# Kernel tuning notes

Measured on AMD Instinct MI355X. Metric: run time of the kernel, lower is better.

Reference implementation:

```python
import jax, jax.numpy as jnp
import numpy as np

# ---- static problem config (matches init_kwargs / input_specs) ----
L = 8                      # num_labels
D = H = W = 96             # volume dims
N = D * H * W
ALPHA, BETA, GAMMA = 8.0, 0.125, 3.0
NIT = 5                    # num_iterations
# 4-D bilateral grid dims: 3 spatial axes scaled by alpha, 1 intensity axis scaled by beta
GD = (int(np.ceil((D - 1) / ALPHA)) + 2,
      int(np.ceil((H - 1) / ALPHA)) + 2,
      int(np.ceil((W - 1) / ALPHA)) + 2,
      int(np.ceil(1.0 / BETA)) + 2)
GSIZE = int(np.prod(GD))
_STRIDES = np.array([GD[1] * GD[2] * GD[3], GD[2] * GD[3], GD[3], 1], dtype=np.int32)


def spatial_gaussian(Q):
    """Exact separable 3D Gaussian filter with sigma=GAMMA. Q: (L, D, H, W)."""
    r = int(3 * GAMMA)
    t = jnp.arange(-r, r + 1, dtype=Q.dtype)
    k = jnp.exp(-0.5 * (t / GAMMA) ** 2)
    k = k / k.sum()
    x = Q[None]  # (1, L, D, H, W)
    for ax in range(3):
        kspatial = [1, 1, 1]
        kspatial[ax] = 2 * r + 1
        kern = jnp.broadcast_to(k.reshape([1, 1] + kspatial), [L, 1] + kspatial)
        pad = [(r, r) if i == ax else (0, 0) for i in range(3)]
        x = jax.lax.conv_general_dilated(
            x, kern, (1, 1, 1), pad, feature_group_count=L,
            dimension_numbers=('NCDHW', 'OIDHW', 'NCDHW'))
    return x[0]


def splat_coords(img):
    """4-D lattice features per voxel. img: (D, H, W). Returns lo (4,N) int32, frac (4,N)."""
    zz, yy, xx = jnp.meshgrid(jnp.arange(D, dtype=img.dtype),
                              jnp.arange(H, dtype=img.dtype),
                              jnp.arange(W, dtype=img.dtype), indexing='ij')
    feats = jnp.stack([zz.reshape(-1) / ALPHA,
                       yy.reshape(-1) / ALPHA,
                       xx.reshape(-1) / ALPHA,
                       img.reshape(-1) / BETA], axis=0)  # (4, N)
    hi = jnp.asarray(GD, feats.dtype).reshape(4, 1) - 2.0
    lo_f = jnp.clip(jnp.floor(feats), 0.0, hi)
    frac = feats - lo_f
    return lo_f.astype(jnp.int32), frac


def blur1(g, ax):
    """[1,2,1]/4 blur along axis ax (grid-unit Gaussian of the splat-blur-slice)."""
    pad = [(0, 0)] * g.ndim
    pad[ax] = (1, 1)
    gp = jnp.pad(g, pad)
    n = g.shape[ax]
    a = jax.lax.slice_in_dim(gp, 0, n, axis=ax)
    b = jax.lax.slice_in_dim(gp, 1, n + 1, axis=ax)
    c = jax.lax.slice_in_dim(gp, 2, n + 2, axis=ax)
    return 0.25 * a + 0.5 * b + 0.25 * c


def lattice_filter(vals, lo, frac):
    """Splat-blur-slice high-dim Gaussian filter. vals: (C, N) -> (C, N)."""
    C = vals.shape[0]
    grid = jnp.zeros((C, GSIZE), vals.dtype)
    idxs, ws = [], []
    for bits in range(16):  # 16 corners of the 4-D cell (multilinear splat)
        off = np.array([(bits >> d) & 1 for d in range(4)], dtype=np.int32)
        w = jnp.prod(jnp.where(off[:, None] == 1, frac, 1.0 - frac), axis=0)  # (N,)
        idx = jnp.sum((lo + off[:, None]) * _STRIDES[:, None], axis=0)        # (N,)
        idxs.append(idx)
        ws.append(w)
        grid = grid.at[:, idx].add(vals * w[None])
    g = grid.reshape((C,) + GD)
    for ax in range(1, 5):
        g = blur1(g, ax)
    gf = g.reshape(C, GSIZE)
    out = jnp.zeros_like(vals)
    for bits in range(16):  # slice
        out = out + ws[bits][None] * gf[:, idxs[bits]]
    return out


def bilateral_apply(Q, lo, frac):
    """Normalized bilateral filtering of Q (L, D, H, W)."""
    vals = jnp.concatenate([Q.reshape(L, N), jnp.ones((1, N), Q.dtype)], axis=0)
    out = lattice_filter(vals, lo, frac)
    return (out[:L] / (out[L:] + 1e-8)).reshape(L, D, H, W)


def reference(U, image, spatial_ker_weights, bilateral_ker_weights, compatibility_matrix):
    Us = U[0]                               # (L, D, H, W); batch must be 1
    lo, frac = splat_coords(image[0, 0])    # lattice built once from image (as in __init__)
    Q = Us
    for _ in range(NIT):
        # NOTE: original code recomputes softmax of the (unchanged) unary U each iteration
        Qsm = jax.nn.softmax(Us, axis=0)
        sp = spatial_gaussian(Qsm).reshape(L, -1)
        bi = bilateral_apply(Qsm, lo, frac).reshape(L, -1)
        Qp = compatibility_matrix @ (spatial_ker_weights @ sp + bilateral_ker_weights @ bi)
        Q = Us + Qp.reshape(L, D, H, W)
    return jax.nn.softmax(Q, axis=0)[None]


def setup_inputs() -> dict:
    key = jax.random.key(0)
    k1, k2 = jax.random.split(key)
    U = jax.random.normal(k1, (1, L, D, H, W), jnp.float32)
    image = jax.random.uniform(k2, (1, 1, D, H, W), jnp.float32)
    eye = jnp.eye(L, dtype=jnp.float32)
    return {
        "U": U,
        "image": image,
        "spatial_ker_weights": 3.0 * eye,     # spatial_ker_weight * I
        "bilateral_ker_weights": 10.0 * eye,  # bilateral_ker_weight * I
        "compatibility_matrix": eye,
    }
```

## Files before the change

kernel.cpp:

```cpp
#include <hip/hip_runtime.h>
#include <math.h>

#define LBL   8
#define DIM   96
#define PLANE (DIM*DIM)
#define NVOX  (DIM*DIM*DIM)
#define GD0 14
#define GD1 14
#define GD2 14
#define GD3 10
#define GSIZE (GD0*GD1*GD2*GD3)
#define ST0 1960
#define ST1 140
#define ST2 10
#define CH  12
#define NBLK 12
#define NBLKS (NBLK*NBLK*NBLK)
#define PART 720
#define GOUT (GSIZE*9)
#define SUP 513
#define ROW8 (DIM/8)
#define PLANE8 (PLANE/8)
#define VOL8 (NVOX/8)
#define XY_BLOCKS 768
#define BLUR_BLOCKS ((GOUT + 255)/256)
#define GRIDF4 (GSIZE*CH/4)

typedef _Float16 half8 __attribute__((ext_vector_type(8)));

__device__ inline half8 h8zero() {
    half8 v;
    #pragma unroll
    for (int e = 0; e < 8; ++e) v[e] = (_Float16)0.f;
    return v;
}

__constant__ float GW[10] = {
    0.13317604f, 0.12597912f, 0.10663904f, 0.08077540f, 0.05475300f,
    0.03320771f, 0.01802341f, 0.00875346f, 0.00380423f, 0.00147945f
};

__global__ __launch_bounds__(512)
void k_zero(float4* __restrict__ g)
{
    const int i = blockIdx.x*512 + threadIdx.x;
    if (i < GRIDF4) {
        float4 z; z.x = 0.f; z.y = 0.f; z.z = 0.f; z.w = 0.f;
        g[i] = z;
    }
}

__global__ __launch_bounds__(512)
void k_softmax_splat(const float* __restrict__ U, const float* __restrict__ img,
                     _Float16* __restrict__ q, float* __restrict__ grid)
{
    __shared__ float sF[512];
    __shared__ __align__(16) unsigned char uball[2880 * 4];
    __shared__ _Float16 sA[64*180];

    _Float16* sU = (_Float16*)uball;
    float*    sB = (float*)uball;

    const int tid = threadIdx.x;
    const int bid0 = blockIdx.x;
    const int bid = (bid0 & 7) * (NBLKS >> 3) + (bid0 >> 3);
    const int bx = bid % NBLK;
    const int by = (bid / NBLK) % NBLK;
    const int bz = bid / (NBLK*NBLK);

    const int lx = tid & 7;
    const int ly = (tid >> 3) & 7;
    const int lz = tid >> 6;

    const int x = bx*8 + lx;
    const int y = by*8 + ly;
    const int z = bz*8 + lz;
    const int vox = z * PLANE + y * DIM + x;

    {
        float u[LBL];
        float m = -1e30f;
        #pragma unroll
        for (int l = 0; l < LBL; ++l) { u[l] = U[l*NVOX + vox]; m = fmaxf(m, u[l]); }
        float ssum = 0.f;
        #pragma unroll
        for (int l = 0; l < LBL; ++l) { u[l] = __expf(u[l] - m); ssum += u[l]; }
        const float inv = 1.f / ssum;
        #pragma unroll
        for (int l = 0; l < LBL; ++l) {
            u[l] *= inv;
            q[l*NVOX + vox] = (_Float16)u[l];
            sU[l*SUP + tid] = (_Float16)u[l];
        }
        sU[8*SUP + tid] = (_Float16)1.0f;
        sF[tid] = img[vox] * 8.0f;
    }
    __syncthreads();

    {
        const int cgrp = tid & 3;
        const int k2   = (tid >> 2) & 1;
        const int row  = tid >> 3;
        const int cb   = cgrp * 2;

        float bins[10][3];
        #pragma unroll
        for (int g = 0; g < 10; ++g) { bins[g][0]=0.f; bins[g][1]=0.f; bins[g][2]=0.f; }

        for (int vx = 0; vx < 8; ++vx) {
            const int vi = row*8 + vx;
            const float f  = sF[vi];
            const float wx = k2 ? (float)vx*0.125f : 1.f - (float)vx*0.125f;
            const float u0 = (float)sU[cb*SUP + vi];
            const float u1 = (float)sU[(cb+1)*SUP + vi];
            const float u2 = (float)sU[8*SUP + vi];
            #pragma unroll
            for (int g = 0; g < 10; ++g) {
                float w = fmaxf(1.f - fabsf(f - (float)g), 0.f) * wx;
                bins[g][0] += w*u0; bins[g][1] += w*u1; bins[g][2] += w*u2;
            }
        }
        _Float16* pA = sA + row*180 + k2*90;
        #pragma unroll
        for (int g = 0; g < 10; ++g) {
            pA[g*9 + cb]     = (_Float16)bins[g][0];
            pA[g*9 + cb + 1] = (_Float16)bins[g][1];
            if (cgrp == 3) pA[g*9 + 8] = (_Float16)bins[g][2];
        }
    }
    __syncthreads();

    if (tid < 288) {
        const int c   = tid % 9;
        const int k2  = (tid / 9) & 1;
        const int j2  = (tid / 18) & 1;
        const int lzo = tid / 36;
        float S[10];
        #pragma unroll
        for (int g = 0; g < 10; ++g) S[g] = 0.f;
        for (int ly2 = 0; ly2 < 8; ++ly2) {
            const float wy = j2 ? (float)ly2*0.125f : 1.f - (float)ly2*0.125f;
            const _Float16* pA = sA + (lzo*8 + ly2)*180 + k2*90;
            #pragma unroll
            for (int g = 0; g < 10; ++g) S[g] += wy * (float)pA[g*9 + c];
        }
        float* pB = sB + lzo*360 + j2*180 + k2*90;
        #pragma unroll
        for (int g = 0; g < 10; ++g) pB[g*9 + c] = S[g];
    }
    __syncthreads();

    for (int item = tid; item < PART; item += 512) {
        const int t  = item / 90;
        const int gc = item % 90;
        const int g  = gc / 9;
        const int c  = gc % 9;
        const int i2 = t >> 2, j2 = (t >> 1) & 1, k2 = t & 1;
        float acc = 0.f;
        #pragma unroll
        for (int lzo = 0; lzo < 8; ++lzo) {
            const float wz = i2 ? (float)lzo*0.125f : 1.f - (float)lzo*0.125f;
            acc += wz * sB[lzo*360 + j2*180 + k2*90 + gc];
        }
        const int cell = (bz + i2)*ST0 + (by + j2)*ST1 + (bx + k2)*ST2 + g;
        atomicAdd(&grid[cell*CH + c], acc);
    }
}

__global__ __launch_bounds__(256)
void k_xy_blur(const half8* __restrict__ src, half8* __restrict__ dst,
               const float* __restrict__ gsrc, float* __restrict__ gdst)
{
    __shared__ _Float16 sIn[PLANE];
    __shared__ _Float16 sX[PLANE];

    const int tid = threadIdx.x;

    if (blockIdx.x >= XY_BLOCKS) {
        const int item = (blockIdx.x - XY_BLOCKS)*256 + tid;
        if (item >= GOUT) return;
        const int c    = item % 9;
        const int cell = item / 9;
        const int gz = cell / ST0;
        int r = cell % ST0;
        const int gy = r / ST1;  r %= ST1;
        const int gx = r / ST2;
        const int g  = r % ST2;

        const int crd[4] = {gz, gy, gx, g};
        const int ext[4] = {GD0, GD1, GD2, GD3};
        const int str[4] = {ST0, ST1, ST2, 1};
        float wa[4][3];
        int   oa[4][3];
        #pragma unroll
        for (int ax = 0; ax < 4; ++ax)
            #pragma unroll
            for (int dd = 0; dd < 3; ++dd) {
                const int cc = crd[ax] + dd - 1;
                const bool ok = (cc >= 0 && cc < ext[ax]);
                wa[ax][dd] = ok ? (dd == 1 ? 0.5f : 0.25f) : 0.f;
                oa[ax][dd] = ok ? (dd - 1) * str[ax] : 0;
            }

        float acc = 0.f;
        #pragma unroll
        for (int a = 0; a < 3; ++a) {
            const float w0 = wa[0][a];
            #pragma unroll
            for (int b = 0; b < 3; ++b) {
                const float w1 = w0 * wa[1][b];
                #pragma unroll
                for (int d2 = 0; d2 < 3; ++d2) {
                    const float w2 = w1 * wa[2][d2];
                    const int ob = oa[0][a] + oa[1][b] + oa[2][d2];
                    #pragma unroll
                    for (int e = 0; e < 3; ++e)
                        acc += w2 * wa[3][e] * gsrc[(cell + ob + oa[3][e])*CH + c];
                }
            }
        }
        gdst[cell*CH + c] = acc;
        return;
    }

    half8* sIn8 = (half8*)sIn;
    half8* sX8  = (half8*)sX;
    const size_t base8 = (size_t)blockIdx.x * PLANE8;

    for (int i = tid; i < PLANE8; i += 256) sIn8[i] = src[base8 + i];
    __syncthreads();

    for (int it = tid; it < 576; it += 256) {
        const int seg = it % 6;
        const int row = it / 6;
        float w[48];
        #pragma unroll
        for (int k = 0; k < 6; ++k) {
            const int j8 = 2*seg - 2 + k;
            half8 v = h8zero();
            if (j8 >= 0 && j8 < ROW8) v = sIn8[row*ROW8 + j8];
            #pragma unroll
            for (int e = 0; e < 8; ++e) w[k*8 + e] = (float)v[e];
        }
        half8 o0 = h8zero(), o1 = h8zero();
        #pragma unroll
        for (int i = 0; i < 16; ++i) {
            float acc = 0.f;
            #pragma unroll
            for (int t = -9; t <= 9; ++t) acc += GW[t < 0 ? -t : t] * w[i + 16 + t];
            if (i < 8) o0[i] = (_Float16)acc; else o1[i - 8] = (_Float16)acc;
        }
        sX8[row*ROW8 + 2*seg]     = o0;
        sX8[row*ROW8 + 2*seg + 1] = o1;
    }
    __syncthreads();

    for (int it = tid; it < 288; it += 256) {
        const int x8   = it % ROW8;
        const int yseg = it / ROW8;
        const int ct = yseg * 4;
        float acc[4][8];
        #pragma unroll
        for (int k = 0; k < 4; ++k)
            #pragma unroll
            for (int e = 0; e < 8; ++e) acc[k][e] = 0.f;
        #pragma unroll
        for (int jj = 0; jj < 22; ++jj) {
            const int j = ct - 9 + jj;
            if (j < 0 || j >= DIM) continue;
            const half8 v = sX8[j*ROW8 + x8];
            float f[8];
            #pragma unroll
            for (int e = 0; e < 8; ++e) f[e] = (float)v[e];
            #pragma unroll
            for (int k = 0; k < 4; ++k) {
                const int d = jj - 9 - k;
                if (d >= -9 && d <= 9) {
                    const float wgt = GW[d < 0 ? -d : d];
                    #pragma unroll
                    for (int e = 0; e < 8; ++e) acc[k][e] += wgt * f[e];
                }
            }
        }
        #pragma unroll
        for (int k = 0; k < 4; ++k) {
            half8 o;
            #pragma unroll
            for (int e = 0; e < 8; ++e) o[e] = (_Float16)acc[k][e];
            dst[base8 + (ct + k)*ROW8 + x8] = o;
        }
    }
}

__global__ __launch_bounds__(256)
void k_gauss_z(const half8* __restrict__ src, half8* __restrict__ dst)
{
    const int bid = blockIdx.x;
    const int swz = (bid & 7) * (864 >> 3) + (bid >> 3);
    const int u = swz * 256 + threadIdx.x;

    const int x8 = u % ROW8;
    const int yy = (u / ROW8) % DIM;
    const int ztl = u / (ROW8 * DIM);
    const int zt = ztl % (DIM/4);
    const int l  = ztl / (DIM/4);
    const int base8 = l * VOL8 + yy * ROW8 + x8;
    const int ct = zt * 4;

    float acc[4][8];
    #pragma unroll
    for (int k = 0; k < 4; ++k)
        #pragma unroll
        for (int e = 0; e < 8; ++e) acc[k][e] = 0.f;

    #pragma unroll
    for (int jj = 0; jj < 22; ++jj) {
        const int j = ct - 9 + jj;
        if (j < 0 || j >= DIM) continue;
        const half8 v = src[base8 + j*PLANE8];
        float f[8];
        #pragma unroll
        for (int e = 0; e < 8; ++e) f[e] = (float)v[e];
        #pragma unroll
        for (int k = 0; k < 4; ++k) {
            const int d = jj - 9 - k;
            if (d >= -9 && d <= 9) {
                const float wgt = GW[d < 0 ? -d : d];
                #pragma unroll
                for (int e = 0; e < 8; ++e) acc[k][e] += wgt * f[e];
            }
        }
    }
    #pragma unroll
    for (int k = 0; k < 4; ++k) {
        half8 o;
        #pragma unroll
        for (int e = 0; e < 8; ++e) o[e] = (_Float16)acc[k][e];
        dst[base8 + (ct + k)*PLANE8] = o;
    }
}

__global__ __launch_bounds__(512)
void k_final(const float* __restrict__ U, const _Float16* __restrict__ sp,
             const float* __restrict__ grid, const float* __restrict__ img,
             const float* __restrict__ Cm, const float* __restrict__ Sw,
             const float* __restrict__ Bw, float* __restrict__ out)
{
    __shared__ float sm[128];
    __shared__ __align__(16) float sG[1800];

    const int tid = threadIdx.x;
    if (tid < 64) {
        const int i = tid >> 3, j = tid & 7;
        float cs = 0.f, cb = 0.f;
        #pragma unroll
        for (int k = 0; k < 8; ++k) {
            cs += Cm[i*8 + k] * Sw[k*8 + j];
            cb += Cm[i*8 + k] * Bw[k*8 + j];
        }
        sm[tid] = cs;
        sm[64 + tid] = cb;
    }

    const int bid0 = blockIdx.x;
    const int bid = (bid0 & 7) * (1728 >> 3) + (bid0 >> 3);
    const int bxi = bid % 3;
    const int byi = (bid / 3) % 6;
    const int z   = bid / 18;

    const int zc0 = z >> 3;
    const float fz = (float)(z & 7) * 0.125f;

    for (int item = tid; item < 1800; item += 512) {
        const int c    = item % 12;
        const int cell = item / 12;
        const int g  = cell % 10;
        const int xc = (cell / 10) % 5;
        const int yc = cell / 50;
        const int cellA = zc0*ST0 + (byi*2 + yc)*ST1 + (bxi*4 + xc)*ST2 + g;
        sG[item] = (1.f - fz)*grid[cellA*CH + c] + fz*grid[(cellA + ST0)*CH + c];
    }
    __syncthreads();

    const int lx  = tid & 31;
    const int lyt = tid >> 5;
    const int x = bxi*32 + lx;
    const int y = byi*16 + lyt;
    const int vox = z*PLANE + y*DIM + x;

    const float f = img[vox] * 8.0f;
    int li = (int)floorf(f);
    li = li < 0 ? 0 : (li > 8 ? 8 : li);
    const float fi = f - (float)li;
    const float fy = (float)(y & 7) * 0.125f;
    const float fx = (float)(x & 7) * 0.125f;
    const float wyv[2] = {1.f - fy, fy};
    const float wxv[2] = {1.f - fx, fx};
    const float wiv[2] = {1.f - fi, fi};
    const int ycb = lyt >> 3;
    const int xcb = lx >> 3;

    float acc[9];
    #pragma unroll
    for (int c = 0; c < 9; ++c) acc[c] = 0.f;

    #pragma unroll
    for (int j2 = 0; j2 < 2; ++j2)
    #pragma unroll
    for (int k2 = 0; k2 < 2; ++k2) {
        const float wsp = wyv[j2] * wxv[k2];
        const int base = (((ycb + j2)*5 + (xcb + k2))*10 + li)*12;
        #pragma unroll
        for (int m2 = 0; m2 < 2; ++m2) {
            const float w = wsp * wiv[m2];
            const float* p = &sG[base + m2*12];
            const float4 p0 = *reinterpret_cast<const float4*>(p);
            const float4 p1 = *reinterpret_cast<const float4*>(p + 4);
            acc[0] += w * p0.x; acc[1] += w * p0.y; acc[2] += w * p0.z; acc[3] += w * p0.w;
            acc[4] += w * p1.x; acc[5] += w * p1.y; acc[6] += w * p1.z; acc[7] += w * p1.w;
            acc[8] += w * p[8];
        }
    }
    const float dinv = 1.f / (acc[8] + 1e-8f);

    float spv[LBL], uu[LBL];
    #pragma unroll
    for (int l = 0; l < LBL; ++l) {
        spv[l] = (float)sp[(size_t)l*NVOX + vox];
        uu[l]  = U[(size_t)l*NVOX + vox];
    }

    float v[LBL];
    float mx = -1e30f;
    #pragma unroll
    for (int i = 0; i < LBL; ++i) {
        float t = 0.f;
        #pragma unroll
        for (int l = 0; l < LBL; ++l)
            t += sm[i*8 + l] * spv[l] + sm[64 + i*8 + l] * (acc[l] * dinv);
        v[i] = uu[i] + t;
        mx = fmaxf(mx, v[i]);
    }
    float ssum = 0.f;
    #pragma unroll
    for (int i = 0; i < LBL; ++i) { v[i] = __expf(v[i] - mx); ssum += v[i]; }
    const float inv = 1.f / ssum;
    #pragma unroll
    for (int i = 0; i < LBL; ++i) out[i*NVOX + vox] = v[i] * inv;
}

extern "C" void kernel_launch(void* const* d_in, const int* in_sizes, int n_in,
                              void* d_out, int out_size, void* d_ws, size_t ws_size,
                              hipStream_t stream)
{
    const float* U   = (const float*)d_in[0];
    const float* img = (const float*)d_in[1];
    const float* Sw  = (const float*)d_in[2];
    const float* Bw  = (const float*)d_in[3];
    const float* Cm  = (const float*)d_in[4];
    float* out = (float*)d_out;

    _Float16* qh  = (_Float16*)d_ws;
    _Float16* g1h = qh + (size_t)LBL * NVOX;
    float* gridA  = (float*)(g1h + (size_t)LBL * NVOX);
    float* gridB  = gridA + (size_t)GSIZE * CH;

    k_zero<<<(GRIDF4 + 511)/512, 512, 0, stream>>>((float4*)gridA);

    k_softmax_splat<<<NBLKS, 512, 0, stream>>>(U, img, qh, gridA);

    k_xy_blur<<<XY_BLOCKS + BLUR_BLOCKS, 256, 0, stream>>>(
        (const half8*)qh, (half8*)g1h, gridA, gridB);

    k_gauss_z<<<864, 256, 0, stream>>>((const half8*)g1h, (half8*)qh);

    k_final<<<1728, 512, 0, stream>>>(U, qh, gridB, img, Cm, Sw, Bw, out);
}
```

Measured before the change: 78.91 us.

## Fuse xy and z Gaussian blurs with counter sync; store fp16 log-softmax

```diff
diff --git a/kernel.cpp b/kernel.cpp
--- a/kernel.cpp
+++ b/kernel.cpp
@@ -23,8 +23,10 @@
 #define PLANE8 (PLANE/8)
 #define VOL8 (NVOX/8)
 #define XY_BLOCKS 768
-#define BLUR_BLOCKS ((GOUT + 255)/256)
+#define ZB 256
 #define GRIDF4 (GSIZE*CH/4)
+#define ZVB 864
+#define BLURVB ((GOUT + 255)/256)
 
 typedef _Float16 half8 __attribute__((ext_vector_type(8)));
 
@@ -41,18 +43,19 @@
 };
 
 __global__ __launch_bounds__(512)
-void k_zero(float4* __restrict__ g)
+void k_zero(float4* __restrict__ g, int* __restrict__ ctr)
 {
     const int i = blockIdx.x*512 + threadIdx.x;
     if (i < GRIDF4) {
         float4 z; z.x = 0.f; z.y = 0.f; z.z = 0.f; z.w = 0.f;
         g[i] = z;
     }
+    if (blockIdx.x == 0 && threadIdx.x < 8) ctr[threadIdx.x] = 0;
 }
 
 __global__ __launch_bounds__(512)
 void k_softmax_splat(const float* __restrict__ U, const float* __restrict__ img,
-                     _Float16* __restrict__ q, float* __restrict__ grid)
+                     _Float16* __restrict__ lnq, float* __restrict__ grid)
 {
     __shared__ float sF[512];
     __shared__ __align__(16) unsigned char uball[2880 * 4];
@@ -78,19 +81,19 @@
     const int vox = z * PLANE + y * DIM + x;
 
     {
-        float u[LBL];
+        float t[LBL], e[LBL];
         float m = -1e30f;
         #pragma unroll
-        for (int l = 0; l < LBL; ++l) { u[l] = U[l*NVOX + vox]; m = fmaxf(m, u[l]); }
+        for (int l = 0; l < LBL; ++l) { t[l] = U[l*NVOX + vox]; m = fmaxf(m, t[l]); }
         float ssum = 0.f;
         #pragma unroll
-        for (int l = 0; l < LBL; ++l) { u[l] = __expf(u[l] - m); ssum += u[l]; }
-        const float inv = 1.f / ssum;
+        for (int l = 0; l < LBL; ++l) { t[l] -= m; e[l] = __expf(t[l]); ssum += e[l]; }
+        const float inv  = 1.f / ssum;
+        const float logs = __logf(ssum);
         #pragma unroll
         for (int l = 0; l < LBL; ++l) {
-            u[l] *= inv;
-            q[l*NVOX + vox] = (_Float16)u[l];
-            sU[l*SUP + tid] = (_Float16)u[l];
+            lnq[l*NVOX + vox] = (_Float16)(t[l] - logs);
+            sU[l*SUP + tid]   = (_Float16)(e[l] * inv);
         }
         sU[8*SUP + tid] = (_Float16)1.0f;
         sF[tid] = img[vox] * 8.0f;
@@ -168,17 +171,105 @@
 }
 
 __global__ __launch_bounds__(256)
-void k_xy_blur(const half8* __restrict__ src, half8* __restrict__ dst,
-               const float* __restrict__ gsrc, float* __restrict__ gdst)
+void k_xyz(const half8* __restrict__ lnq, half8* __restrict__ g1,
+           half8* __restrict__ sp,
+           const float* __restrict__ gsrc, float* __restrict__ gdst,
+           int* __restrict__ ctr)
 {
     __shared__ _Float16 sIn[PLANE];
     __shared__ _Float16 sX[PLANE];
 
     const int tid = threadIdx.x;
-
-    if (blockIdx.x >= XY_BLOCKS) {
-        const int item = (blockIdx.x - XY_BLOCKS)*256 + tid;
-        if (item >= GOUT) return;
+    const int bid = blockIdx.x;
+
+    if (bid < XY_BLOCKS) {
+        half8* sIn8 = (half8*)sIn;
+        half8* sX8  = (half8*)sX;
+        const size_t base8 = (size_t)bid * PLANE8;
+
+        for (int i = tid; i < PLANE8; i += 256) {
+            const half8 v = lnq[base8 + i];
+            half8 w;
+            #pragma unroll
+            for (int e = 0; e < 8; ++e) w[e] = (_Float16)__expf((float)v[e]);
+            sIn8[i] = w;
+        }
+        __syncthreads();
+
+        for (int it = tid; it < 576; it += 256) {
+            const int seg = it % 6;
+            const int row = it / 6;
+            float w[48];
+            #pragma unroll
+            for (int k = 0; k < 6; ++k) {
+                const int j8 = 2*seg - 2 + k;
+                half8 v = h8zero();
+                if (j8 >= 0 && j8 < ROW8) v = sIn8[row*ROW8 + j8];
+                #pragma unroll
+                for (int e = 0; e < 8; ++e) w[k*8 + e] = (float)v[e];
+            }
+            half8 o0 = h8zero(), o1 = h8zero();
+            #pragma unroll
+            for (int i = 0; i < 16; ++i) {
+                float acc = 0.f;
+                #pragma unroll
+                for (int t = -9; t <= 9; ++t) acc += GW[t < 0 ? -t : t] * w[i + 16 + t];
+                if (i < 8) o0[i] = (_Float16)acc; else o1[i - 8] = (_Float16)acc;
+            }
+            sX8[row*ROW8 + 2*seg]     = o0;
+            sX8[row*ROW8 + 2*seg + 1] = o1;
+        }
+        __syncthreads();
+
+        for (int it = tid; it < 288; it += 256) {
+            const int x8   = it % ROW8;
+            const int yseg = it / ROW8;
+            const int ct = yseg * 4;
+            float acc[4][8];
+            #pragma unroll
+            for (int k = 0; k < 4; ++k)
+                #pragma unroll
+                for (int e = 0; e < 8; ++e) acc[k][e] = 0.f;
+            #pragma unroll
+            for (int jj = 0; jj < 22; ++jj) {
+                const int j = ct - 9 + jj;
+                if (j < 0 || j >= DIM) continue;
+                const half8 v = sX8[j*ROW8 + x8];
+                float f[8];
+                #pragma unroll
+                for (int e = 0; e < 8; ++e) f[e] = (float)v[e];
+                #pragma unroll
+                for (int k = 0; k < 4; ++k) {
+                    const int d = jj - 9 - k;
+                    if (d >= -9 && d <= 9) {
+                        const float wgt = GW[d < 0 ? -d : d];
+                        #pragma unroll
+                        for (int e = 0; e < 8; ++e) acc[k][e] += wgt * f[e];
+                    }
+                }
+            }
+            #pragma unroll
+            for (int k = 0; k < 4; ++k) {
+                half8 o;
+                #pragma unroll
+                for (int e = 0; e < 8; ++e) o[e] = (_Float16)acc[k][e];
+                g1[base8 + (ct + k)*ROW8 + x8] = o;
+            }
+        }
+
+        __threadfence();
+        __syncthreads();
+        if (tid == 0)
+            __hip_atomic_fetch_add(&ctr[bid / 96], 1,
+                                   __ATOMIC_RELEASE, __HIP_MEMORY_SCOPE_AGENT);
+        return;
+    }
+
+    const int zbid = bid - XY_BLOCKS;
+
+    for (int vb = zbid; vb < BLURVB; vb += ZB) {
+        const int item = vb*256 + tid;
+        if (item >= GOUT) continue;
         const int c    = item % 9;
         const int cell = item / 9;
         const int gz = cell / ST0;
@@ -201,7 +292,6 @@
                 wa[ax][dd] = ok ? (dd == 1 ? 0.5f : 0.25f) : 0.f;
                 oa[ax][dd] = ok ? (dd - 1) * str[ax] : 0;
             }
-
         float acc = 0.f;
         #pragma unroll
         for (int a = 0; a < 3; ++a) {
@@ -220,55 +310,38 @@
             }
         }
         gdst[cell*CH + c] = acc;
-        return;
-    }
-
-    half8* sIn8 = (half8*)sIn;
-    half8* sX8  = (half8*)sX;
-    const size_t base8 = (size_t)blockIdx.x * PLANE8;
-
-    for (int i = tid; i < PLANE8; i += 256) sIn8[i] = src[base8 + i];
-    __syncthreads();
-
-    for (int it = tid; it < 576; it += 256) {
-        const int seg = it % 6;
-        const int row = it / 6;
-        float w[48];
-        #pragma unroll
-        for (int k = 0; k < 6; ++k) {
-            const int j8 = 2*seg - 2 + k;
-            half8 v = h8zero();
-            if (j8 >= 0 && j8 < ROW8) v = sIn8[row*ROW8 + j8];
-            #pragma unroll
-            for (int e = 0; e < 8; ++e) w[k*8 + e] = (float)v[e];
-        }
-        half8 o0 = h8zero(), o1 = h8zero();
-        #pragma unroll
-        for (int i = 0; i < 16; ++i) {
-            float acc = 0.f;
-            #pragma unroll
-            for (int t = -9; t <= 9; ++t) acc += GW[t < 0 ? -t : t] * w[i + 16 + t];
-            if (i < 8) o0[i] = (_Float16)acc; else o1[i - 8] = (_Float16)acc;
-        }
-        sX8[row*ROW8 + 2*seg]     = o0;
-        sX8[row*ROW8 + 2*seg + 1] = o1;
-    }
-    __syncthreads();
-
-    for (int it = tid; it < 288; it += 256) {
-        const int x8   = it % ROW8;
-        const int yseg = it / ROW8;
-        const int ct = yseg * 4;
+    }
+
+    for (int vb = zbid; vb < ZVB; vb += ZB) {
+        const int lw = vb / 108;
+        if (tid == 0) {
+            while (__hip_atomic_load(&ctr[lw], __ATOMIC_ACQUIRE,
+                                     __HIP_MEMORY_SCOPE_AGENT) < 96)
+                __builtin_amdgcn_s_sleep(8);
+        }
+        __syncthreads();
+        __threadfence();
+
+        const int u = vb*256 + tid;
+        const int x8 = u % ROW8;
+        const int yy = (u / ROW8) % DIM;
+        const int ztl = u / (ROW8 * DIM);
+        const int zt = ztl % (DIM/4);
+        const int l  = ztl / (DIM/4);
+        const int base8 = l * VOL8 + yy * ROW8 + x8;
+        const int ct = zt * 4;
+
         float acc[4][8];
         #pragma unroll
         for (int k = 0; k < 4; ++k)
             #pragma unroll
             for (int e = 0; e < 8; ++e) acc[k][e] = 0.f;
+
         #pragma unroll
         for (int jj = 0; jj < 22; ++jj) {
             const int j = ct - 9 + jj;
             if (j < 0 || j >= DIM) continue;
-            const half8 v = sX8[j*ROW8 + x8];
+            const half8 v = g1[base8 + j*PLANE8];
             float f[8];
             #pragma unroll
             for (int e = 0; e < 8; ++e) f[e] = (float)v[e];
@@ -287,61 +360,13 @@
             half8 o;
             #pragma unroll
             for (int e = 0; e < 8; ++e) o[e] = (_Float16)acc[k][e];
-            dst[base8 + (ct + k)*ROW8 + x8] = o;
+            sp[base8 + (ct + k)*PLANE8] = o;
         }
     }
 }
 
-__global__ __launch_bounds__(256)
-void k_gauss_z(const half8* __restrict__ src, half8* __restrict__ dst)
-{
-    const int bid = blockIdx.x;
-    const int swz = (bid & 7) * (864 >> 3) + (bid >> 3);
-    const int u = swz * 256 + threadIdx.x;
-
-    const int x8 = u % ROW8;
-    const int yy = (u / ROW8) % DIM;
-    const int ztl = u / (ROW8 * DIM);
-    const int zt = ztl % (DIM/4);
-    const int l  = ztl / (DIM/4);
-    const int base8 = l * VOL8 + yy * ROW8 + x8;
-    const int ct = zt * 4;
-
-    float acc[4][8];
-    #pragma unroll
-    for (int k = 0; k < 4; ++k)
-        #pragma unroll
-        for (int e = 0; e < 8; ++e) acc[k][e] = 0.f;
-
-    #pragma unroll
-    for (int jj = 0; jj < 22; ++jj) {
-        const int j = ct - 9 + jj;
-        if (j < 0 || j >= DIM) continue;
-        const half8 v = src[base8 + j*PLANE8];
-        float f[8];
-        #pragma unroll
-        for (int e = 0; e < 8; ++e) f[e] = (float)v[e];
-        #pragma unroll
-        for (int k = 0; k < 4; ++k) {
-            const int d = jj - 9 - k;
-            if (d >= -9 && d <= 9) {
-                const float wgt = GW[d < 0 ? -d : d];
-                #pragma unroll
-                for (int e = 0; e < 8; ++e) acc[k][e] += wgt * f[e];
-            }
-        }
-    }
-    #pragma unroll
-    for (int k = 0; k < 4; ++k) {
-        half8 o;
-        #pragma unroll
-        for (int e = 0; e < 8; ++e) o[e] = (_Float16)acc[k][e];
-        dst[base8 + (ct + k)*PLANE8] = o;
-    }
-}
-
 __global__ __launch_bounds__(512)
-void k_final(const float* __restrict__ U, const _Float16* __restrict__ sp,
+void k_final(const _Float16* __restrict__ lnq, const _Float16* __restrict__ sp,
              const float* __restrict__ grid, const float* __restrict__ img,
              const float* __restrict__ Cm, const float* __restrict__ Sw,
              const float* __restrict__ Bw, float* __restrict__ out)
@@ -423,11 +448,11 @@
     }
     const float dinv = 1.f / (acc[8] + 1e-8f);
 
-    float spv[LBL], uu[LBL];
+    float spv[LBL], lq[LBL];
     #pragma unroll
     for (int l = 0; l < LBL; ++l) {
         spv[l] = (float)sp[(size_t)l*NVOX + vox];
-        uu[l]  = U[(size_t)l*NVOX + vox];
+        lq[l]  = (float)lnq[(size_t)l*NVOX + vox];
     }
 
     float v[LBL];
@@ -438,7 +463,7 @@
         #pragma unroll
         for (int l = 0; l < LBL; ++l)
             t += sm[i*8 + l] * spv[l] + sm[64 + i*8 + l] * (acc[l] * dinv);
-        v[i] = uu[i] + t;
+        v[i] = lq[i] + t;
         mx = fmaxf(mx, v[i]);
     }
     float ssum = 0.f;
@@ -461,18 +486,18 @@
     float* out = (float*)d_out;
 
     _Float16* qh  = (_Float16*)d_ws;
-    _Float16* g1h = qh + (size_t)LBL * NVOX;
-    float* gridA  = (float*)(g1h + (size_t)LBL * NVOX);
+    _Float16* g1h = qh  + (size_t)LBL * NVOX;
+    _Float16* g2h = g1h + (size_t)LBL * NVOX;
+    float* gridA  = (float*)(g2h + (size_t)LBL * NVOX);
     float* gridB  = gridA + (size_t)GSIZE * CH;
-
-    k_zero<<<(GRIDF4 + 511)/512, 512, 0, stream>>>((float4*)gridA);
+    int*   ctr    = (int*)(gridB + (size_t)GSIZE * CH);
+
+    k_zero<<<(GRIDF4 + 511)/512, 512, 0, stream>>>((float4*)gridA, ctr);
 
     k_softmax_splat<<<NBLKS, 512, 0, stream>>>(U, img, qh, gridA);
 
-    k_xy_blur<<<XY_BLOCKS + BLUR_BLOCKS, 256, 0, stream>>>(
-        (const half8*)qh, (half8*)g1h, gridA, gridB);
-
-    k_gauss_z<<<864, 256, 0, stream>>>((const half8*)g1h, (half8*)qh);
-
-    k_final<<<1728, 512, 0, stream>>>(U, qh, gridB, img, Cm, Sw, Bw, out);
+    k_xyz<<<XY_BLOCKS + ZB, 256, 0, stream>>>(
+        (const half8*)qh, (half8*)g1h, (half8*)g2h, gridA, gridB, ctr);
+
+    k_final<<<1728, 512, 0, stream>>>(qh, g2h, gridB, img, Cm, Sw, Bw, out);
 }
```

Result: slower. 288.0 us (+265.1%).
